# Kernel tuning notes

Measured on AMD Instinct MI355X. Metric: run time of the kernel, lower is better.

Reference implementation:

```python
import jax, jax.numpy as jnp
import numpy as np


def setup_inputs() -> dict:
    key = jax.random.key(0)
    k1, k2, k3, k4 = jax.random.split(key, 4)
    B, C, L = 16, 512, 4096
    x = jax.random.normal(k1, (B, C, L), dtype=jnp.float32)
    # conv1d kernel_size=1, bias=False -> weight [3C, C]
    w_qkv = jax.random.normal(k2, (3 * C, C), dtype=jnp.float32) * (1.0 / np.sqrt(C))
    w_out = jax.random.normal(k3, (C, C), dtype=jnp.float32) * (1.0 / np.sqrt(C))
    b_out = jax.random.normal(k4, (C,), dtype=jnp.float32) * 0.01
    return {"x": x, "w_qkv": w_qkv, "w_out": w_out, "b_out": b_out}


def reference(x, w_qkv, w_out, b_out):
    # x: [b, c, l]; 1x1 conv == channel-wise matmul
    qkv = jnp.einsum('bcl,oc->bol', x, w_qkv)          # [b, 3c, l]
    q, k, v = jnp.split(qkv, 3, axis=1)                 # each [b, c, l] (heads=1)
    k = jax.nn.softmax(k, axis=-1)                      # softmax over sequence dim l
    context = jnp.einsum('bdn,ben->bde', k, v)          # [b, c, c]
    out = jnp.einsum('bde,bdn->ben', context, q)        # [b, c, l]
    return jnp.einsum('bcl,oc->bol', out, w_out) + b_out[None, :, None]
```

## Files before the change

kernel.cpp:

```cpp
#include <hip/hip_runtime.h>
#include <hip/hip_bf16.h>
#include <type_traits>

#define DEVINL __device__ __forceinline__

typedef float f32x4 __attribute__((ext_vector_type(4)));
typedef __bf16 bf16x8 __attribute__((ext_vector_type(8)));

DEVINL float bf2f(short s) {
  unsigned u = ((unsigned)(unsigned short)s) << 16;
  float f; __builtin_memcpy(&f, &u, 4); return f;
}
DEVINL short f2bf(float f) {
  unsigned u; __builtin_memcpy(&u, &f, 4);
  u += 0x7fff + ((u >> 16) & 1);
  return (short)(u >> 16);
}

DEVINL void gl_lds16(const void* g, void* l) {
  __builtin_amdgcn_global_load_lds(
      (const __attribute__((address_space(1))) void*)g,
      (__attribute__((address_space(3))) void*)l, 16, 0, 0);
}

template <typename OutT, bool BIAS>
DEVINL void epilogue_store(f32x4 (&acc)[4][4], char* smem,
                           OutT* __restrict__ C, int ldc, int m0, int n0,
                           const float* __restrict__ bias, int t) {
  const int wave = t >> 6, lane = t & 63;
  const int quad = lane >> 4, l16 = lane & 15;
  const int arow = (wave >> 1) * 64, brow = (wave & 1) * 64;
  if constexpr (std::is_same<OutT, float>::value) {
    float* tile = (float*)smem;
#pragma unroll
    for (int rnd = 0; rnd < 2; ++rnd) {
      if ((arow >> 6) == rnd) {
#pragma unroll
        for (int mi = 0; mi < 4; ++mi)
#pragma unroll
          for (int ni = 0; ni < 4; ++ni) {
            const int col = brow + ni * 16 + l16;
#pragma unroll
            for (int r = 0; r < 4; ++r) {
              const int row = mi * 16 + quad * 4 + r;
              float v = acc[mi][ni][r];
              if (BIAS) v += bias[m0 + rnd * 64 + row];
              tile[row * 128 + col] = v;
            }
          }
      }
      __syncthreads();
#pragma unroll
      for (int i = 0; i < 8; ++i) {
        const int row = wave * 16 + i * 2 + (lane >> 5);
        const int cf  = (lane & 31) * 4;
        f32x4 v = *(f32x4*)&tile[row * 128 + cf];
        *(f32x4*)&C[(long)(m0 + rnd * 64 + row) * ldc + n0 + cf] = v;
      }
      __syncthreads();
    }
  } else {
    short* tile = (short*)smem;
#pragma unroll
    for (int mi = 0; mi < 4; ++mi)
#pragma unroll
      for (int ni = 0; ni < 4; ++ni) {
        const int col = brow + ni * 16 + l16;
#pragma unroll
        for (int r = 0; r < 4; ++r) {
          const int row = arow + mi * 16 + quad * 4 + r;
          float v = acc[mi][ni][r];
          if (BIAS) v += bias[m0 + row];
          tile[row * 128 + col] = f2bf(v);
        }
      }
    __syncthreads();
#pragma unroll
    for (int i = 0; i < 8; ++i) {
      const int row = wave * 32 + i * 4 + (lane >> 4);
      const int cs  = l16 * 8;
      int4 v = *(int4*)&tile[row * 128 + cs];
      *(int4*)&C[(long)(m0 + row) * ldc + n0 + cs] = v;
    }
  }
}

template <typename OutT, bool BIAS>
__global__ __launch_bounds__(256)
void gemm_nt(const short* __restrict__ A, long sA, int lda,
             const short* __restrict__ B, long sB, int ldb,
             OutT* __restrict__ C, long sC, int ldc,
             const float* __restrict__ bias, int K)
{
  A += (long)blockIdx.z * sA;
  B += (long)blockIdx.z * sB;
  C += (long)blockIdx.z * sC;

  __shared__ char smem[32768];
  short* As = (short*)smem;
  short* Bs = (short*)(smem + 8192);

  const int t    = threadIdx.x;
  const int wave = t >> 6, lane = t & 63;
  const int quad = lane >> 4, l16 = lane & 15;
  const int m0 = blockIdx.y * 128, n0 = blockIdx.x * 128;
  const int lrow = t >> 2;
  const int lk8  = (t & 3) * 8;
  const int arow = (wave >> 1) * 64, brow = (wave & 1) * 64;

  f32x4 acc[4][4];
#pragma unroll
  for (int i = 0; i < 4; ++i)
#pragma unroll
    for (int j = 0; j < 4; ++j) acc[i][j] = (f32x4){0.f, 0.f, 0.f, 0.f};

  for (int k0 = 0; k0 < K; k0 += 32) {
#pragma unroll
    for (int s = 0; s < 2; ++s) {
      gl_lds16(A + (long)(m0 + s * 64 + lrow) * lda + k0 + lk8,
               (char*)As + s * 4096 + wave * 1024);
      gl_lds16(B + (long)(n0 + s * 64 + lrow) * ldb + k0 + lk8,
               (char*)Bs + s * 4096 + wave * 1024);
    }
    __syncthreads();

    bf16x8 af[4], bfr[4];
#pragma unroll
    for (int i = 0; i < 4; ++i)
      af[i] = *(const bf16x8*)&As[(arow + i * 16 + l16) * 32 + quad * 8];
#pragma unroll
    for (int i = 0; i < 4; ++i)
      bfr[i] = *(const bf16x8*)&Bs[(brow + i * 16 + l16) * 32 + quad * 8];

#pragma unroll
    for (int mi = 0; mi < 4; ++mi)
#pragma unroll
      for (int ni = 0; ni < 4; ++ni)
        acc[mi][ni] = __builtin_amdgcn_mfma_f32_16x16x32_bf16(
            af[mi], bfr[ni], acc[mi][ni], 0, 0, 0);
    __syncthreads();
  }

  epilogue_store<OutT, BIAS>(acc, smem, C, ldc, m0, n0, bias, t);
}

__global__ __launch_bounds__(256)
void gemm_ctx_sk(const short* __restrict__ kv, float* __restrict__ ctxp)
{
  const int b = blockIdx.z >> 2, s = blockIdx.z & 3;
  const short* A = kv + (long)b * 4194304;
  const short* B = kv + (long)b * 4194304 + 2097152;
  float* Cp = ctxp + (long)(s * 16 + b) * 262144;

  __shared__ char smem[32768];
  short* As = (short*)smem;
  short* Bs = (short*)(smem + 8192);

  const int t    = threadIdx.x;
  const int wave = t >> 6, lane = t & 63;
  const int quad = lane >> 4, l16 = lane & 15;
  const int m0 = blockIdx.y * 128, n0 = blockIdx.x * 128;
  const int lrow = t >> 2;
  const int lk8  = (t & 3) * 8;
  const int arow = (wave >> 1) * 64, brow = (wave & 1) * 64;
  const int kbeg = s * 1024, kend = kbeg + 1024;

  f32x4 acc[4][4];
#pragma unroll
  for (int i = 0; i < 4; ++i)
#pragma unroll
    for (int j = 0; j < 4; ++j) acc[i][j] = (f32x4){0.f, 0.f, 0.f, 0.f};

  for (int k0 = kbeg; k0 < kend; k0 += 32) {
#pragma unroll
    for (int sb = 0; sb < 2; ++sb) {
      gl_lds16(A + (long)(m0 + sb * 64 + lrow) * 4096 + k0 + lk8,
               (char*)As + sb * 4096 + wave * 1024);
      gl_lds16(B + (long)(n0 + sb * 64 + lrow) * 4096 + k0 + lk8,
               (char*)Bs + sb * 4096 + wave * 1024);
    }
    __syncthreads();

    bf16x8 af[4], bfr[4];
#pragma unroll
    for (int i = 0; i < 4; ++i)
      af[i] = *(const bf16x8*)&As[(arow + i * 16 + l16) * 32 + quad * 8];
#pragma unroll
    for (int i = 0; i < 4; ++i)
      bfr[i] = *(const bf16x8*)&Bs[(brow + i * 16 + l16) * 32 + quad * 8];

#pragma unroll
    for (int mi = 0; mi < 4; ++mi)
#pragma unroll
      for (int ni = 0; ni < 4; ++ni)
        acc[mi][ni] = __builtin_amdgcn_mfma_f32_16x16x32_bf16(
            af[mi], bfr[ni], acc[mi][ni], 0, 0, 0);
    __syncthreads();
  }

  epilogue_store<float, false>(acc, smem, Cp, 512, m0, n0, nullptr, t);
}

__global__ void reduce_ctx(const float* __restrict__ ctxp, short* __restrict__ ctx) {
  const long i = ((long)blockIdx.x * 256 + threadIdx.x) * 4;
  f32x4 a = *(const f32x4*)&ctxp[i];
  f32x4 b = *(const f32x4*)&ctxp[i + 4194304];
  f32x4 c = *(const f32x4*)&ctxp[i + 2 * 4194304];
  f32x4 d = *(const f32x4*)&ctxp[i + 3 * 4194304];
  short o[4];
#pragma unroll
  for (int j = 0; j < 4; ++j) o[j] = f2bf(a[j] + b[j] + c[j] + d[j]);
  *(long*)&ctx[i] = *(long*)o;
}

DEVINL float to_f(float v) { return v; }
DEVINL float to_f(short v) { return bf2f(v); }

template <typename InT, typename OutT>
__global__ void transpose_k(const InT* __restrict__ src, OutT* __restrict__ dst,
                            int R, int Cc, long ss, long ds)
{
  __shared__ float tile[32][33];
  src += (long)blockIdx.z * ss;
  dst += (long)blockIdx.z * ds;
  const int c0 = blockIdx.x * 32, r0 = blockIdx.y * 32;
  const int tx = threadIdx.x, ty = threadIdx.y;
#pragma unroll
  for (int i = 0; i < 4; ++i)
    tile[ty + i * 8][tx] = to_f(src[(long)(r0 + ty + i * 8) * Cc + c0 + tx]);
  __syncthreads();
#pragma unroll
  for (int i = 0; i < 4; ++i) {
    float v = tile[tx][ty + i * 8];
    if constexpr (std::is_same<OutT, float>::value)
      dst[(long)(c0 + ty + i * 8) * R + r0 + tx] = v;
    else
      dst[(long)(c0 + ty + i * 8) * R + r0 + tx] = f2bf(v);
  }
}

__global__ void cast_weights(const float* __restrict__ wq, short* __restrict__ wqb,
                             const float* __restrict__ wo, short* __restrict__ wob) {
  const int i = blockIdx.x * 256 + threadIdx.x;
  if (i < 786432) wqb[i] = f2bf(wq[i]);
  else            wob[i - 786432] = f2bf(wo[i - 786432]);
}

__global__ void softmax_rows(short* __restrict__ kv) {
  const int b = blockIdx.x >> 9, d = blockIdx.x & 511;
  short* p = kv + (long)b * 4194304 + (long)d * 4096;
  const int t = threadIdx.x, wave = t >> 6, lane = t & 63;

  short v16[16];
  *(int4*)&v16[0] = *(const int4*)&p[t * 8];
  *(int4*)&v16[8] = *(const int4*)&p[2048 + t * 8];

  float vals[16];
  float m = -1e30f;
#pragma unroll
  for (int i = 0; i < 16; ++i) {
    vals[i] = bf2f(v16[i]);
    m = fmaxf(m, vals[i]);
  }
  for (int off = 32; off; off >>= 1) m = fmaxf(m, __shfl_xor(m, off));
  __shared__ float redm[4], reds[4];
  if (lane == 0) redm[wave] = m;
  __syncthreads();
  m = fmaxf(fmaxf(redm[0], redm[1]), fmaxf(redm[2], redm[3]));

  float s = 0.f;
#pragma unroll
  for (int i = 0; i < 16; ++i) { vals[i] = __expf(vals[i] - m); s += vals[i]; }
  for (int off = 32; off; off >>= 1) s += __shfl_xor(s, off);
  if (lane == 0) reds[wave] = s;
  __syncthreads();
  s = reds[0] + reds[1] + reds[2] + reds[3];
  const float inv = 1.f / s;
#pragma unroll
  for (int i = 0; i < 16; ++i) v16[i] = f2bf(vals[i] * inv);
  *(int4*)&p[t * 8] = *(int4*)&v16[0];
  *(int4*)&p[2048 + t * 8] = *(int4*)&v16[8];
}

extern "C" void kernel_launch(void* const* d_in, const int* in_sizes, int n_in,
                              void* d_out, int out_size, void* d_ws, size_t ws_size,
                              hipStream_t stream) {
  const float* x     = (const float*)d_in[0];
  const float* w_qkv = (const float*)d_in[1];
  const float* w_out = (const float*)d_in[2];
  const float* b_out = (const float*)d_in[3];
  float* out = (float*)d_out;

  const long CL = (long)512 * 4096;
  const long KV = (long)1024 * 4096;
  const long CC = (long)512 * 512;

  char* ws = (char*)d_ws;
  short* xT   = (short*)(ws);
  short* kv   = (short*)(ws + 67108864);
  float* ctxp = (float*)(ws + 201326592);
  short* ctx  = (short*)(ws + 268435456);
  short* M2   = (short*)(ws + 276824064);
  short* M3   = (short*)(ws + 285212672);
  short* wqb  = (short*)(ws + 293601280);
  short* wob  = (short*)(ws + 295174144);
  short* wqT  = (short*)(ws + 295698432);

  cast_weights<<<4096, 256, 0, stream>>>(w_qkv, wqb, w_out, wob);

  transpose_k<float, short><<<dim3(16, 16, 1), dim3(32, 8), 0, stream>>>(
      w_qkv, wqT, 512, 512, 0, 0);

  transpose_k<float, short><<<dim3(128, 16, 16), dim3(32, 8), 0, stream>>>(
      x, xT, 512, 4096, CL, CL);

  gemm_nt<short, false><<<dim3(32, 8, 16), 256, 0, stream>>>(
      wqb + 512 * 512, 0, 512, xT, CL, 512, kv, KV, 4096, nullptr, 512);

  softmax_rows<<<16 * 512, 256, 0, stream>>>(kv);

  gemm_ctx_sk<<<dim3(4, 4, 64), 256, 0, stream>>>(kv, ctxp);
  reduce_ctx<<<4096, 256, 0, stream>>>(ctxp, ctx);

  gemm_nt<short, false><<<dim3(4, 4, 16), 256, 0, stream>>>(
      wob, 0, 512, ctx, CC, 512, M2, CC, 512, nullptr, 512);

  gemm_nt<short, false><<<dim3(4, 4, 16), 256, 0, stream>>>(
      M2, CC, 512, wqT, 0, 512, M3, CC, 512, nullptr, 512);

  gemm_nt<float, true><<<dim3(32, 4, 16), 256, 0, stream>>>(
      M3, CC, 512, xT, CL, 512, out, CL, 4096, b_out, 512);
}
```

Baseline: 562.4 us.

## Compute context as softmax(K)·Xᵀ then multiply by Wvᵀ instead of materializing V

Instead of projecting V over the whole sequence, the context is computed as P = softmax(K)·Xᵀ (a bf16 copy of x is produced inside a fused transpose+cast kernel), and then multiplied by the V weight slice with a small 512x512 GEMM per batch. This removes the large V projection GEMM and halves the projected activation buffer, replacing it with a cheap per-batch GEMM. It also adds an occupancy hint to the GEMM launch bounds. The fused transpose now writes two bf16 copies of x, adding some memory traffic.

Result: faster. 533.2 us (-5.2%).

```diff
diff --git a/kernel.cpp b/kernel.cpp
--- a/kernel.cpp
+++ b/kernel.cpp
@@ -86,7 +86,7 @@
 }
 
 template <typename OutT, bool BIAS>
-__global__ __launch_bounds__(256)
+__global__ __launch_bounds__(256, 4)
 void gemm_nt(const short* __restrict__ A, long sA, int lda,
              const short* __restrict__ B, long sB, int ldb,
              OutT* __restrict__ C, long sC, int ldc,
@@ -144,13 +144,14 @@
   epilogue_store<OutT, BIAS>(acc, smem, C, ldc, m0, n0, bias, t);
 }
 
-__global__ __launch_bounds__(256)
-void gemm_ctx_sk(const short* __restrict__ kv, float* __restrict__ ctxp)
+__global__ __launch_bounds__(256, 4)
+void gemm_sk(const short* __restrict__ Ab, const short* __restrict__ Bb,
+             float* __restrict__ Cp)
 {
   const int b = blockIdx.z >> 2, s = blockIdx.z & 3;
-  const short* A = kv + (long)b * 4194304;
-  const short* B = kv + (long)b * 4194304 + 2097152;
-  float* Cp = ctxp + (long)(s * 16 + b) * 262144;
+  const short* A = Ab + (long)b * 2097152;
+  const short* B = Bb + (long)b * 2097152;
+  float* C = Cp + (long)(s * 16 + b) * 262144;
 
   __shared__ char smem[32768];
   short* As = (short*)smem;
@@ -198,19 +199,40 @@
     __syncthreads();
   }
 
-  epilogue_store<float, false>(acc, smem, Cp, 512, m0, n0, nullptr, t);
-}
-
-__global__ void reduce_ctx(const float* __restrict__ ctxp, short* __restrict__ ctx) {
+  epilogue_store<float, false>(acc, smem, C, 512, m0, n0, nullptr, t);
+}
+
+__global__ void reduce_sk(const float* __restrict__ p, short* __restrict__ o) {
   const long i = ((long)blockIdx.x * 256 + threadIdx.x) * 4;
-  f32x4 a = *(const f32x4*)&ctxp[i];
-  f32x4 b = *(const f32x4*)&ctxp[i + 4194304];
-  f32x4 c = *(const f32x4*)&ctxp[i + 2 * 4194304];
-  f32x4 d = *(const f32x4*)&ctxp[i + 3 * 4194304];
-  short o[4];
-#pragma unroll
-  for (int j = 0; j < 4; ++j) o[j] = f2bf(a[j] + b[j] + c[j] + d[j]);
-  *(long*)&ctx[i] = *(long*)o;
+  f32x4 a = *(const f32x4*)&p[i];
+  f32x4 b = *(const f32x4*)&p[i + 4194304];
+  f32x4 c = *(const f32x4*)&p[i + 2 * 4194304];
+  f32x4 d = *(const f32x4*)&p[i + 3 * 4194304];
+  short r[4];
+#pragma unroll
+  for (int j = 0; j < 4; ++j) r[j] = f2bf(a[j] + b[j] + c[j] + d[j]);
+  *(long*)&o[i] = *(long*)r;
+}
+
+__global__ void transpose_cast(const float* __restrict__ x,
+                               short* __restrict__ xT, short* __restrict__ xb)
+{
+  __shared__ float tile[32][33];
+  x  += (long)blockIdx.z * 2097152;
+  xT += (long)blockIdx.z * 2097152;
+  xb += (long)blockIdx.z * 2097152;
+  const int l0 = blockIdx.x * 32, c0 = blockIdx.y * 32;
+  const int tx = threadIdx.x, ty = threadIdx.y;
+#pragma unroll
+  for (int i = 0; i < 4; ++i) {
+    float v = x[(long)(c0 + ty + i * 8) * 4096 + l0 + tx];
+    tile[ty + i * 8][tx] = v;
+    xb[(long)(c0 + ty + i * 8) * 4096 + l0 + tx] = f2bf(v);
+  }
+  __syncthreads();
+#pragma unroll
+  for (int i = 0; i < 4; ++i)
+    xT[(long)(l0 + ty + i * 8) * 512 + c0 + tx] = f2bf(tile[tx][ty + i * 8]);
 }
 
 DEVINL float to_f(float v) { return v; }
@@ -246,9 +268,9 @@
   else            wob[i - 786432] = f2bf(wo[i - 786432]);
 }
 
-__global__ void softmax_rows(short* __restrict__ kv) {
+__global__ void softmax_rows(short* __restrict__ k) {
   const int b = blockIdx.x >> 9, d = blockIdx.x & 511;
-  short* p = kv + (long)b * 4194304 + (long)d * 4096;
+  short* p = k + (long)b * 2097152 + (long)d * 4096;
   const int t = threadIdx.x, wave = t >> 6, lane = t & 63;
 
   short v16[16];
@@ -292,35 +314,38 @@
   float* out = (float*)d_out;
 
   const long CL = (long)512 * 4096;
-  const long KV = (long)1024 * 4096;
   const long CC = (long)512 * 512;
 
   char* ws = (char*)d_ws;
-  short* xT   = (short*)(ws);
-  short* kv   = (short*)(ws + 67108864);
-  float* ctxp = (float*)(ws + 201326592);
-  short* ctx  = (short*)(ws + 268435456);
-  short* M2   = (short*)(ws + 276824064);
-  short* M3   = (short*)(ws + 285212672);
-  short* wqb  = (short*)(ws + 293601280);
-  short* wob  = (short*)(ws + 295174144);
-  short* wqT  = (short*)(ws + 295698432);
+  short* xT  = (short*)(ws);
+  short* xb  = (short*)(ws + 67108864);
+  short* kbf = (short*)(ws + 134217728);
+  float* Pp  = (float*)(ws + 201326592);
+  short* P   = (short*)(ws + 268435456);
+  short* ctx = (short*)(ws + 276824064);
+  short* M2  = (short*)(ws + 285212672);
+  short* M3  = (short*)(ws + 293601280);
+  short* wqb = (short*)(ws + 301989888);
+  short* wob = (short*)(ws + 303562752);
+  short* wqT = (short*)(ws + 304087040);
 
   cast_weights<<<4096, 256, 0, stream>>>(w_qkv, wqb, w_out, wob);
 
   transpose_k<float, short><<<dim3(16, 16, 1), dim3(32, 8), 0, stream>>>(
       w_qkv, wqT, 512, 512, 0, 0);
 
-  transpose_k<float, short><<<dim3(128, 16, 16), dim3(32, 8), 0, stream>>>(
-      x, xT, 512, 4096, CL, CL);
-
-  gemm_nt<short, false><<<dim3(32, 8, 16), 256, 0, stream>>>(
-      wqb + 512 * 512, 0, 512, xT, CL, 512, kv, KV, 4096, nullptr, 512);
-
-  softmax_rows<<<16 * 512, 256, 0, stream>>>(kv);
-
-  gemm_ctx_sk<<<dim3(4, 4, 64), 256, 0, stream>>>(kv, ctxp);
-  reduce_ctx<<<4096, 256, 0, stream>>>(ctxp, ctx);
+  transpose_cast<<<dim3(128, 16, 16), dim3(32, 8), 0, stream>>>(x, xT, xb);
+
+  gemm_nt<short, false><<<dim3(32, 4, 16), 256, 0, stream>>>(
+      wqb + 512 * 512, 0, 512, xT, CL, 512, kbf, CL, 4096, nullptr, 512);
+
+  softmax_rows<<<16 * 512, 256, 0, stream>>>(kbf);
+
+  gemm_sk<<<dim3(4, 4, 64), 256, 0, stream>>>(kbf, xb, Pp);
+  reduce_sk<<<4096, 256, 0, stream>>>(Pp, P);
+
+  gemm_nt<short, false><<<dim3(4, 4, 16), 256, 0, stream>>>(
+      P, CC, 512, wqb + 2 * 512 * 512, 0, 512, ctx, CC, 512, nullptr, 512);
 
   gemm_nt<short, false><<<dim3(4, 4, 16), 256, 0, stream>>>(
       wob, 0, 512, ctx, CC, 512, M2, CC, 512, nullptr, 512);
```
